# Optimization experiments

Measured on AMD Instinct MI355X. Metric: run time of the kernel, lower is better.

Reference implementation:

```python
import jax, jax.numpy as jnp
import numpy as np

B = 1024            # number of graphs
C = (64, 32, 16, 1) # args.channels
K = 25              # args.kernel_size
CUTOFF = 0.5        # args.cutoff
EPS = 1e-15


def gmm_conv(x, pos, n, g, mu, sigma, root, bias, out_ch):
    """GMMConv over a dynamically-built radius graph (dist<CUTOFF, no self loops),
    with mean aggregation, expressed densely per-graph (n in {5,25,75}).
    Equivalent to getA()+PyG GMMConv(aggr='mean') scatter/gather."""
    nb = pos.shape[0] // n
    posb = pos.reshape(nb, n, 2)
    # diff[b, s, t] = pos_t - pos_s  (edge (row=s, col=t): message flows s -> t)
    diff = posb[:, None, :, :] - posb[:, :, None, :]
    dist = jnp.linalg.norm(diff + 1e-12, axis=-1)            # [B,n,n]
    mask = (dist < CUTOFF) & (~jnp.eye(n, dtype=bool))       # [B,n,n]
    pseudo = diff / CUTOFF + 0.5                             # [B,n,n,2] edge_attr
    # Gaussian kernel weights: exp(-0.5 * sum_d (u_d - mu_kd)^2 / sigma_kd^2)
    gauss = jnp.exp(-0.5 * jnp.sum((pseudo[..., None, :] - mu) ** 2
                                   / (sigma ** 2 + EPS), axis=-1))  # [B,n,n,K]
    w = gauss * mask[..., None]
    xm = (x @ g).reshape(nb, n, K, out_ch)                   # source-transformed feats
    agg = jnp.einsum('bstk,bsko->bto', w, xm)                # scatter-sum into targets
    deg = jnp.maximum(jnp.sum(mask, axis=1), 1)              # in-degree per target [B,n]
    out = agg / deg[..., None].astype(x.dtype)               # mean aggregation
    return out.reshape(-1, out_ch) + x @ root + bias


def setup_inputs() -> dict:
    key = jax.random.key(0)
    ks = jax.random.split(key, 40)
    inp = {}
    inp['x'] = jax.random.normal(ks[0], (B * 5, C[0]), jnp.float32)
    inp['pos'] = jax.random.uniform(ks[1], (B * 5, 2), jnp.float32)

    def conv_params(k, fin, fout):
        k1, k2, k3, k4, k5 = jax.random.split(k, 5)
        g = jax.random.normal(k1, (fin, K * fout), jnp.float32) / np.sqrt(fin)
        mu = jax.random.normal(k2, (K, 2), jnp.float32)
        sigma = jax.random.uniform(k3, (K, 2), jnp.float32, minval=0.5, maxval=1.5)
        root = jax.random.normal(k4, (fin, fout), jnp.float32) / np.sqrt(fin)
        bias = jax.random.normal(k5, (fout,), jnp.float32) * 0.01
        return g, mu, sigma, root, bias

    for i, (fin, fout) in enumerate([(C[0], 5 * C[1]), (C[1], 3 * C[2]), (C[2], C[3])], 1):
        g, mu, sigma, root, bias = conv_params(ks[1 + i], fin, fout)
        inp[f'g{i}'], inp[f'mu{i}'], inp[f'sig{i}'] = g, mu, sigma
        inp[f'root{i}'], inp[f'cb{i}'] = root, bias

    def lin(k, fin, fout):
        kw, kb = jax.random.split(k)
        return (jax.random.normal(kw, (fin, fout), jnp.float32) / np.sqrt(fin),
                jax.random.normal(kb, (fout,), jnp.float32) * 0.01)

    for j, (pre, dims) in enumerate([('p1', (2 + C[1], 128, 64, 2)),
                                     ('p2', (2 + C[2], 128, 64, 2))]):
        for li in range(3):
            w, b_ = lin(ks[10 + 3 * j + li], dims[li], dims[li + 1])
            inp[f'{pre}w{li+1}'], inp[f'{pre}b{li+1}'] = w, b_
    return inp


def reference(x, pos, g1, mu1, sig1, root1, cb1, g2, mu2, sig2, root2, cb2,
              g3, mu3, sig3, root3, cb3,
              p1w1, p1b1, p1w2, p1b2, p1w3, p1b3,
              p2w1, p2b1, p2w2, p2b2, p2w3, p2b3):
    elu = jax.nn.elu
    # stage 1: 5 nodes/graph, conv expands node count x5
    x = elu(gmm_conv(x, pos, 5, g1, mu1, sig1, root1, cb1, 5 * C[1])).reshape(-1, C[1])
    p = jnp.concatenate([jnp.repeat(pos, 5, axis=0), x], axis=1)
    p = elu(p @ p1w1 + p1b1)
    p = elu(p @ p1w2 + p1b2)
    pos = elu(p @ p1w3 + p1b3)
    # stage 2: 25 nodes/graph, conv expands node count x3
    x = elu(gmm_conv(x, pos, 25, g2, mu2, sig2, root2, cb2, 3 * C[2])).reshape(-1, C[2])
    p = jnp.concatenate([jnp.repeat(pos, 3, axis=0), x], axis=1)
    p = elu(p @ p2w1 + p2b1)
    p = elu(p @ p2w2 + p2b2)
    pos = elu(p @ p2w3 + p2b3)
    # stage 3: 75 nodes/graph
    x = jnp.tanh(gmm_conv(x, pos, 75, g3, mu3, sig3, root3, cb3, C[3])).reshape(-1, C[3])
    return x, pos
```

## Files before the change

### kernel.cpp

```cpp
#include <hip/hip_runtime.h>
#include <math.h>


__device__ __forceinline__ float eluf(float v) { return v > 0.f ? v : __expf(v) - 1.f; }

#define NLOG2E_HALF (-0.72134752f)

__global__ __launch_bounds__(512) void conv1_kernel(
    const float* __restrict__ x, const float* __restrict__ pos,
    const float* __restrict__ g, const float* __restrict__ mu, const float* __restrict__ sig,
    const float* __restrict__ root, const float* __restrict__ bias,
    float* __restrict__ xout)
{
  const int b = blockIdx.x, tid = threadIdx.x;
  __shared__ __align__(16) float s_xT[64 * 12];
  __shared__ __align__(16) float s_xm[10 * 832];
  __shared__ __align__(16) float s_w[2 * 5 * 5 * 28];
  __shared__ __align__(16) float s_red[2 * 2 * 5 * 160];
  __shared__ float s_pos[20];
  __shared__ float s_msc[25][4];
  __shared__ float s_ideg[10];

  if (tid < 20) s_pos[tid] = pos[b * 20 + tid];
  if (tid < 25) {
    float m0 = mu[2 * tid], m1 = mu[2 * tid + 1];
    float s0 = sig[2 * tid], s1 = sig[2 * tid + 1];
    s_msc[tid][0] = 0.5f - m0;
    s_msc[tid][1] = 0.5f - m1;
    s_msc[tid][2] = NLOG2E_HALF / (s0 * s0 + 1e-15f);
    s_msc[tid][3] = NLOG2E_HALF / (s1 * s1 + 1e-15f);
  }
  for (int e = tid; e < 640; e += 512) { int nd = e >> 6, i = e & 63; s_xT[i * 12 + nd] = x[b * 640 + nd * 64 + i]; }
  for (int e = tid; e < 320; e += 512) { int r = e / 32, c = e % 32; s_xm[r * 832 + 800 + c] = 0.f; }
  __syncthreads();

  if (tid < 10) {
    int gg = tid / 5, t = tid % 5, c = 0;
    for (int s = 0; s < 5; ++s) {
      if (s == t) continue;
      float d0 = s_pos[(gg * 5 + t) * 2]     - s_pos[(gg * 5 + s) * 2]     + 1e-12f;
      float d1 = s_pos[(gg * 5 + t) * 2 + 1] - s_pos[(gg * 5 + s) * 2 + 1] + 1e-12f;
      c += (d0 * d0 + d1 * d1 < 0.25f) ? 1 : 0;
    }
    s_ideg[tid] = 1.f / (float)(c < 1 ? 1 : c);
  }
  for (int e = tid; e < 1400; e += 512) {
    int gg = e / 700, r2 = e % 700, t = r2 / 140, c = r2 % 140;
    int ch = c / 28, skl = c % 28;
    float wv = 0.f;
    if (skl < 25) {
      int kk = skl / 5, s = skl % 5, k = ch * 5 + kk;
      float d0 = s_pos[(gg * 5 + t) * 2]     - s_pos[(gg * 5 + s) * 2];
      float d1 = s_pos[(gg * 5 + t) * 2 + 1] - s_pos[(gg * 5 + s) * 2 + 1];
      float e0 = d0 + 1e-12f, e1 = d1 + 1e-12f;
      bool m = (e0 * e0 + e1 * e1 < 0.25f) && (s != t);
      float q0 = fmaf(2.f, d0, s_msc[k][0]);
      float q1 = fmaf(2.f, d1, s_msc[k][1]);
      float a = q0 * q0 * s_msc[k][2];
      a = fmaf(q1 * q1, s_msc[k][3], a);
      wv = m ? exp2f(a) : 0.f;
    }
    s_w[e] = wv;
  }
  __syncthreads();

  float sacc[5][2];
  #pragma unroll
  for (int t = 0; t < 5; ++t) { sacc[t][0] = 0.f; sacc[t][1] = 0.f; }
  const int sg = tid / 160, sr = tid % 160, sks = sr / 80, sob = sr % 80;
  const int so0 = sob * 2;

  for (int ch = 0; ch < 5; ++ch) {
    if (tid < 400) {
      const int c0 = tid * 2;
      const float* gp = g + ch * 800 + c0;
      float a[10][2];
      #pragma unroll
      for (int r = 0; r < 10; ++r) { a[r][0] = 0.f; a[r][1] = 0.f; }
      #pragma unroll 4
      for (int i = 0; i < 64; ++i) {
        float2 gv = *(const float2*)(gp + i * 4000);
        float4 xa = *(const float4*)&s_xT[i * 12];
        float4 xb = *(const float4*)&s_xT[i * 12 + 4];
        float2 xc = *(const float2*)&s_xT[i * 12 + 8];
        a[0][0] = fmaf(xa.x, gv.x, a[0][0]); a[0][1] = fmaf(xa.x, gv.y, a[0][1]);
        a[1][0] = fmaf(xa.y, gv.x, a[1][0]); a[1][1] = fmaf(xa.y, gv.y, a[1][1]);
        a[2][0] = fmaf(xa.z, gv.x, a[2][0]); a[2][1] = fmaf(xa.z, gv.y, a[2][1]);
        a[3][0] = fmaf(xa.w, gv.x, a[3][0]); a[3][1] = fmaf(xa.w, gv.y, a[3][1]);
        a[4][0] = fmaf(xb.x, gv.x, a[4][0]); a[4][1] = fmaf(xb.x, gv.y, a[4][1]);
        a[5][0] = fmaf(xb.y, gv.x, a[5][0]); a[5][1] = fmaf(xb.y, gv.y, a[5][1]);
        a[6][0] = fmaf(xb.z, gv.x, a[6][0]); a[6][1] = fmaf(xb.z, gv.y, a[6][1]);
        a[7][0] = fmaf(xb.w, gv.x, a[7][0]); a[7][1] = fmaf(xb.w, gv.y, a[7][1]);
        a[8][0] = fmaf(xc.x, gv.x, a[8][0]); a[8][1] = fmaf(xc.x, gv.y, a[8][1]);
        a[9][0] = fmaf(xc.y, gv.x, a[9][0]); a[9][1] = fmaf(xc.y, gv.y, a[9][1]);
      }
      #pragma unroll
      for (int r = 0; r < 10; ++r)
        *(float2*)&s_xm[r * 832 + c0] = make_float2(a[r][0], a[r][1]);
    }
    __syncthreads();
    if (tid < 320) {
#define C1_STEP(SK0) { \
      float2 m0 = *(const float2*)&s_xm[(sg * 5 + ((SK0) % 5)) * 832 + ((SK0) / 5) * 160 + so0]; \
      float2 m1 = *(const float2*)&s_xm[(sg * 5 + (((SK0) + 1) % 5)) * 832 + (((SK0) + 1) / 5) * 160 + so0]; \
      float2 m2 = *(const float2*)&s_xm[(sg * 5 + (((SK0) + 2) % 5)) * 832 + (((SK0) + 2) / 5) * 160 + so0]; \
      float2 m3 = *(const float2*)&s_xm[(sg * 5 + (((SK0) + 3) % 5)) * 832 + (((SK0) + 3) / 5) * 160 + so0]; \
      _Pragma("unroll") \
      for (int t = 0; t < 5; ++t) { \
        const float4 wv = *(const float4*)&s_w[((sg * 5 + t) * 5 + ch) * 28 + (SK0)]; \
        sacc[t][0] = fmaf(wv.x, m0.x, sacc[t][0]); sacc[t][1] = fmaf(wv.x, m0.y, sacc[t][1]); \
        sacc[t][0] = fmaf(wv.y, m1.x, sacc[t][0]); sacc[t][1] = fmaf(wv.y, m1.y, sacc[t][1]); \
        sacc[t][0] = fmaf(wv.z, m2.x, sacc[t][0]); sacc[t][1] = fmaf(wv.z, m2.y, sacc[t][1]); \
        sacc[t][0] = fmaf(wv.w, m3.x, sacc[t][0]); sacc[t][1] = fmaf(wv.w, m3.y, sacc[t][1]); \
      } }
      if (sks == 0) { C1_STEP(0) C1_STEP(4) C1_STEP(8) C1_STEP(12) }
      else          { C1_STEP(16) C1_STEP(20) C1_STEP(24) }
#undef C1_STEP
    }
    __syncthreads();
  }

  if (tid < 400) {
    const int rb = tid / 80, cb = tid % 80;
    const int r0 = rb * 2, c0 = cb * 2;
    float a00 = 0.f, a01 = 0.f, a10 = 0.f, a11 = 0.f;
    #pragma unroll 4
    for (int i = 0; i < 64; ++i) {
      float2 rv = *(const float2*)(root + i * 160 + c0);
      float2 xv = *(const float2*)&s_xT[i * 12 + r0];
      a00 = fmaf(xv.x, rv.x, a00); a01 = fmaf(xv.x, rv.y, a01);
      a10 = fmaf(xv.y, rv.x, a10); a11 = fmaf(xv.y, rv.y, a11);
    }
    *(float2*)&s_xm[r0 * 832 + c0]       = make_float2(a00, a01);
    *(float2*)&s_xm[(r0 + 1) * 832 + c0] = make_float2(a10, a11);
  }
  if (tid < 320) {
    #pragma unroll
    for (int t = 0; t < 5; ++t) {
      s_red[((sks * 2 + sg) * 5 + t) * 160 + so0]     = sacc[t][0];
      s_red[((sks * 2 + sg) * 5 + t) * 160 + so0 + 1] = sacc[t][1];
    }
  }
  __syncthreads();
  for (int e = tid; e < 1600; e += 512) {
    int gg = e / 800, r2 = e % 800, t = r2 / 160, o = r2 % 160;
    float v = s_red[(gg * 5 + t) * 160 + o] + s_red[((2 + gg) * 5 + t) * 160 + o];
    v = v * s_ideg[gg * 5 + t] + s_xm[(gg * 5 + t) * 832 + o] + bias[o];
    xout[b * 1600 + e] = eluf(v);
  }
}

__global__ __launch_bounds__(320) void conv2_kernel(
    const float* __restrict__ x, const float* __restrict__ pos,
    const float* __restrict__ g, const float* __restrict__ mu, const float* __restrict__ sig,
    const float* __restrict__ root, const float* __restrict__ bias,
    float* __restrict__ xout)
{
  const int b = blockIdx.x, tid = threadIdx.x;
  __shared__ __align__(16) float s_xT[32 * 28];
  __shared__ __align__(16) float s_xm[125 * 52];
  __shared__ __align__(16) float s_w[25 * 132];
  __shared__ __align__(8)  float2 s_u[25 * 26];
  __shared__ float s_ek[25 * 5];
  __shared__ float s_pos[50];
  __shared__ float s_ideg[25];

  if (tid < 50) s_pos[tid] = pos[b * 50 + tid];
  if (tid < 25) {
    float m0 = mu[2 * tid], m1 = mu[2 * tid + 1];
    float sg0 = sig[2 * tid], sg1 = sig[2 * tid + 1];
    float n0 = NLOG2E_HALF / (sg0 * sg0 + 1e-15f);
    float n1 = NLOG2E_HALF / (sg1 * sg1 + 1e-15f);
    float c0 = 0.5f - m0, c1 = 0.5f - m1;
    s_ek[tid * 5 + 0] = n0;
    s_ek[tid * 5 + 1] = n1;
    s_ek[tid * 5 + 2] = 2.f * n0 * c0;
    s_ek[tid * 5 + 3] = 2.f * n1 * c1;
    s_ek[tid * 5 + 4] = fmaf(n0, c0 * c0, n1 * c1 * c1);
  }
  for (int e = tid; e < 800; e += 320) { int r = e / 32, i = e % 32; s_xT[i * 28 + r] = x[b * 800 + e]; }
  __syncthreads();

  for (int e = tid; e < 625; e += 320) {
    int t = e / 25, s = e % 25;
    float d0 = s_pos[t * 2]     - s_pos[s * 2];
    float d1 = s_pos[t * 2 + 1] - s_pos[s * 2 + 1];
    float e0 = d0 + 1e-12f, e1 = d1 + 1e-12f;
    bool m = (e0 * e0 + e1 * e1 < 0.25f) && (s != t);
    s_u[t * 26 + s] = m ? make_float2(2.f * d0, 2.f * d1) : make_float2(1e18f, 0.f);
  }
  if (tid < 25) {
    int t = tid, c = 0;
    for (int s = 0; s < 25; ++s) {
      if (s == t) continue;
      float d0 = s_pos[t * 2]     - s_pos[s * 2]     + 1e-12f;
      float d1 = s_pos[t * 2 + 1] - s_pos[s * 2 + 1] + 1e-12f;
      c += (d0 * d0 + d1 * d1 < 0.25f) ? 1 : 0;
    }
    s_ideg[t] = 1.f / (float)(c < 1 ? 1 : c);
  }
  __syncthreads();

  const bool act = tid < 300;
  const int grp = tid / 60, rr = tid % 60, tg = rr / 12, og = rr % 12;
  const int o0 = og * 4;
  const int t0 = tg * 5, sk0 = grp * 25, s0 = tg * 5;

  float acc2[5][4];
  #pragma unroll
  for (int tt = 0; tt < 5; ++tt) { acc2[tt][0] = acc2[tt][1] = acc2[tt][2] = acc2[tt][3] = 0.f; }

  for (int ch = 0; ch < 5; ++ch) {
    const int k0 = ch * 5;
    for (int e = tid; e < 3125; e += 320) {
      int t = e / 125, c = e % 125;
      int kk = c / 25, s = c % 25, k = k0 + kk;
      float2 uv = s_u[t * 26 + s];
      const float* ekp = &s_ek[k * 5];
      float ar = fmaf(uv.x * uv.x, ekp[0],
                 fmaf(uv.y * uv.y, ekp[1],
                 fmaf(uv.x, ekp[2],
                 fmaf(uv.y, ekp[3], ekp[4]))));
      s_w[t * 132 + c] = exp2f(ar);
    }
    if (act) {
      const float* gp = g + (k0 + grp) * 48 + o0;
      float a[5][4];
      #pragma unroll
      for (int r = 0; r < 5; ++r) { a[r][0] = a[r][1] = a[r][2] = a[r][3] = 0.f; }
      #pragma unroll 4
      for (int i = 0; i < 32; ++i) {
        float4 gv = *(const float4*)(gp + i * 1200);
        float x0 = s_xT[i * 28 + s0];
        float x1 = s_xT[i * 28 + s0 + 1];
        float x2 = s_xT[i * 28 + s0 + 2];
        float x3 = s_xT[i * 28 + s0 + 3];
        float x4 = s_xT[i * 28 + s0 + 4];
        a[0][0] = fmaf(x0, gv.x, a[0][0]); a[0][1] = fmaf(x0, gv.y, a[0][1]);
        a[0][2] = fmaf(x0, gv.z, a[0][2]); a[0][3] = fmaf(x0, gv.w, a[0][3]);
        a[1][0] = fmaf(x1, gv.x, a[1][0]); a[1][1] = fmaf(x1, gv.y, a[1][1]);
        a[1][2] = fmaf(x1, gv.z, a[1][2]); a[1][3] = fmaf(x1, gv.w, a[1][3]);
        a[2][0] = fmaf(x2, gv.x, a[2][0]); a[2][1] = fmaf(x2, gv.y, a[2][1]);
        a[2][2] = fmaf(x2, gv.z, a[2][2]); a[2][3] = fmaf(x2, gv.w, a[2][3]);
        a[3][0] = fmaf(x3, gv.x, a[3][0]); a[3][1] = fmaf(x3, gv.y, a[3][1]);
        a[3][2] = fmaf(x3, gv.z, a[3][2]); a[3][3] = fmaf(x3, gv.w, a[3][3]);
        a[4][0] = fmaf(x4, gv.x, a[4][0]); a[4][1] = fmaf(x4, gv.y, a[4][1]);
        a[4][2] = fmaf(x4, gv.z, a[4][2]); a[4][3] = fmaf(x4, gv.w, a[4][3]);
      }
      #pragma unroll
      for (int j = 0; j < 5; ++j)
        *(float4*)&s_xm[(grp * 25 + s0 + j) * 52 + o0] = make_float4(a[j][0], a[j][1], a[j][2], a[j][3]);
    }
    __syncthreads();
    if (act) {
      #pragma unroll 5
      for (int q = 0; q < 25; ++q) {
        const int sk = sk0 + q;
        float4 mv = *(const float4*)&s_xm[sk * 52 + o0];
        float w0 = s_w[(t0 + 0) * 132 + sk];
        float w1 = s_w[(t0 + 1) * 132 + sk];
        float w2 = s_w[(t0 + 2) * 132 + sk];
        float w3 = s_w[(t0 + 3) * 132 + sk];
        float w4 = s_w[(t0 + 4) * 132 + sk];
        acc2[0][0] = fmaf(w0, mv.x, acc2[0][0]); acc2[0][1] = fmaf(w0, mv.y, acc2[0][1]);
        acc2[0][2] = fmaf(w0, mv.z, acc2[0][2]); acc2[0][3] = fmaf(w0, mv.w, acc2[0][3]);
        acc2[1][0] = fmaf(w1, mv.x, acc2[1][0]); acc2[1][1] = fmaf(w1, mv.y, acc2[1][1]);
        acc2[1][2] = fmaf(w1, mv.z, acc2[1][2]); acc2[1][3] = fmaf(w1, mv.w, acc2[1][3]);
        acc2[2][0] = fmaf(w2, mv.x, acc2[2][0]); acc2[2][1] = fmaf(w2, mv.y, acc2[2][1]);
        acc2[2][2] = fmaf(w2, mv.z, acc2[2][2]); acc2[2][3] = fmaf(w2, mv.w, acc2[2][3]);
        acc2[3][0] = fmaf(w3, mv.x, acc2[3][0]); acc2[3][1] = fmaf(w3, mv.y, acc2[3][1]);
        acc2[3][2] = fmaf(w3, mv.z, acc2[3][2]); acc2[3][3] = fmaf(w3, mv.w, acc2[3][3]);
        acc2[4][0] = fmaf(w4, mv.x, acc2[4][0]); acc2[4][1] = fmaf(w4, mv.y, acc2[4][1]);
        acc2[4][2] = fmaf(w4, mv.z, acc2[4][2]); acc2[4][3] = fmaf(w4, mv.w, acc2[4][3]);
      }
    }
    __syncthreads();
  }

  if (act) {
    #pragma unroll
    for (int tt = 0; tt < 5; ++tt)
      *(float4*)&s_xm[grp * 1200 + (t0 + tt) * 48 + o0] =
          make_float4(acc2[tt][0], acc2[tt][1], acc2[tt][2], acc2[tt][3]);
  }
  __syncthreads();
  for (int e = tid; e < 1200; e += 320) {
    int t = e / 48, o = e % 48;
    float v = s_xm[e] + s_xm[1200 + e] + s_xm[2400 + e] + s_xm[3600 + e] + s_xm[4800 + e];
    v *= s_ideg[t];
    #pragma unroll 8
    for (int i = 0; i < 32; ++i) v = fmaf(s_xT[i * 28 + t], root[i * 48 + o], v);
    xout[b * 1200 + e] = eluf(v + bias[o]);
  }
}

__global__ __launch_bounds__(384) void conv3_kernel(
    const float* __restrict__ x, const float* __restrict__ pos,
    const float* __restrict__ g, const float* __restrict__ mu, const float* __restrict__ sig,
    const float* __restrict__ root, const float* __restrict__ bias,
    float* __restrict__ xout)
{
  const int b = blockIdx.x, tid = threadIdx.x;
  __shared__ __align__(8) float2 s_u[75 * 75];
  __shared__ float s_xm[75 * 28];
  __shared__ float s_x[75 * 16];
  __shared__ float s_g3[400];
  __shared__ float s_pos[150];
  __shared__ float s_ek[25 * 5];
  __shared__ float s_ideg[75];
  __shared__ float s_out[75];
  __shared__ float s_r3[16];

  if (tid < 150) s_pos[tid] = pos[b * 150 + tid];
  for (int e = tid; e < 1200; e += 384) s_x[e] = x[b * 1200 + e];
  for (int e = tid; e < 400; e += 384) s_g3[e] = g[e];
  if (tid < 25) {
    float m0 = mu[2 * tid], m1 = mu[2 * tid + 1];
    float sg0 = sig[2 * tid], sg1 = sig[2 * tid + 1];
    float n0 = NLOG2E_HALF / (sg0 * sg0 + 1e-15f);
    float n1 = NLOG2E_HALF / (sg1 * sg1 + 1e-15f);
    float c0 = 0.5f - m0, c1 = 0.5f - m1;
    s_ek[tid * 5 + 0] = n0;
    s_ek[tid * 5 + 1] = n1;
    s_ek[tid * 5 + 2] = 2.f * n0 * c0;
    s_ek[tid * 5 + 3] = 2.f * n1 * c1;
    s_ek[tid * 5 + 4] = n0 * c0 * c0 + n1 * c1 * c1;
  }
  if (tid < 16) s_r3[tid] = root[tid];
  if (tid < 75) s_out[tid] = 0.f;
  __syncthreads();

  for (int e = tid; e < 1875; e += 384) {
    int s = e / 25, k = e % 25;
    float a = 0.f;
    #pragma unroll
    for (int i = 0; i < 16; ++i) a = fmaf(s_x[s * 16 + i], s_g3[i * 25 + k], a);
    s_xm[s * 28 + k] = a;
  }
  for (int e = tid; e < 5625; e += 384) {
    int t = e / 75, s = e % 75;
    float d0 = s_pos[t * 2]     - s_pos[s * 2];
    float d1 = s_pos[t * 2 + 1] - s_pos[s * 2 + 1];
    float e0 = d0 + 1e-12f, e1 = d1 + 1e-12f;
    bool m = (e0 * e0 + e1 * e1 < 0.25f) && (s != t);
    s_u[e] = m ? make_float2(2.f * d0, 2.f * d1) : make_float2(1e18f, 0.f);
  }
  if (tid < 75) {
    int t = tid, c = 0;
    for (int s = 0; s < 75; ++s) {
      if (s == t) continue;
      float d0 = s_pos[t * 2]     - s_pos[s * 2]     + 1e-12f;
      float d1 = s_pos[t * 2 + 1] - s_pos[s * 2 + 1] + 1e-12f;
      c += (d0 * d0 + d1 * d1 < 0.25f) ? 1 : 0;
    }
    s_ideg[t] = 1.f / (float)(c < 1 ? 1 : c);
  }
  __syncthreads();

  if (tid < 375) {
    const int t = tid / 5, kg = tid % 5;
    float n0[5], n1[5], e0[5], e1[5], f[5];
    #pragma unroll
    for (int j = 0; j < 5; ++j) {
      int k = kg * 5 + j;
      n0[j] = s_ek[k * 5 + 0]; n1[j] = s_ek[k * 5 + 1];
      e0[j] = s_ek[k * 5 + 2]; e1[j] = s_ek[k * 5 + 3];
      f[j]  = s_ek[k * 5 + 4];
    }
    float acc[5] = {0.f, 0.f, 0.f, 0.f, 0.f};
    for (int s = 0; s < 75; ++s) {
      float2 uv = s_u[t * 75 + s];
      float u00 = uv.x * uv.x, u11 = uv.y * uv.y;
      #pragma unroll
      for (int j = 0; j < 5; ++j) {
        float ar = fmaf(u00, n0[j], fmaf(u11, n1[j], fmaf(uv.x, e0[j], fmaf(uv.y, e1[j], f[j]))));
        acc[j] = fmaf(exp2f(ar), s_xm[s * 28 + kg * 5 + j], acc[j]);
      }
    }
    float sum = acc[0] + acc[1] + acc[2] + acc[3] + acc[4];
    atomicAdd(&s_out[t], sum);
  }
  __syncthreads();

  if (tid < 75) {
    int t = tid;
    float r = 0.f;
    #pragma unroll
    for (int i = 0; i < 16; ++i) r = fmaf(s_x[t * 16 + i], s_r3[i], r);
    xout[b * 75 + t] = tanhf(s_out[t] * s_ideg[t] + r + bias[0]);
  }
}

__global__ __launch_bounds__(256) void mlp_kernel(
    const float* __restrict__ pos_src, const float* __restrict__ feat,
    const float* __restrict__ w1, const float* __restrict__ b1,
    const float* __restrict__ w2, const float* __restrict__ b2,
    const float* __restrict__ w3, const float* __restrict__ b3,
    float* __restrict__ out, int fdim, int rep)
{
  const int tid = threadIdx.x;
  const int row0 = blockIdx.x * 64;
  const int din = fdim + 2;
  __shared__ __align__(16) float s_inT[34][68];
  __shared__ __align__(16) float s_h1T[128][68];
  __shared__ __align__(16) float s_h2T[64][68];

  if (tid < 128) {
    int r = tid >> 1, d = tid & 1;
    s_inT[d][r] = pos_src[((row0 + r) / rep) * 2 + d];
  }
  for (int e = tid; e < 64 * fdim; e += 256) {
    int r = e / fdim, c = e % fdim;
    s_inT[2 + c][r] = feat[(row0 + r) * fdim + c];
  }
  __syncthreads();

  {
    const int rb = tid >> 4, jb = tid & 15;
    const int r0 = rb << 2, j0 = jb << 3;
    float acc[4][8];
    #pragma unroll
    for (int jj = 0; jj < 8; ++jj) {
      float bv = b1[j0 + jj];
      acc[0][jj] = bv; acc[1][jj] = bv; acc[2][jj] = bv; acc[3][jj] = bv;
    }
    for (int i = 0; i < din; ++i) {
      float4 xa = *(const float4*)&s_inT[i][r0];
      float4 wa = *(const float4*)(w1 + i * 128 + j0);
      float4 wb = *(const float4*)(w1 + i * 128 + j0 + 4);
      float wv[8] = {wa.x, wa.y, wa.z, wa.w, wb.x, wb.y, wb.z, wb.w};
      #pragma unroll
      for (int jj = 0; jj < 8; ++jj) {
        acc[0][jj] = fmaf(xa.x, wv[jj], acc[0][jj]);
        acc[1][jj] = fmaf(xa.y, wv[jj], acc[1][jj]);
        acc[2][jj] = fmaf(xa.z, wv[jj], acc[2][jj]);
        acc[3][jj] = fmaf(xa.w, wv[jj], acc[3][jj]);
      }
    }
    #pragma unroll
    for (int jj = 0; jj < 8; ++jj)
      *(float4*)&s_h1T[j0 + jj][r0] =
        make_float4(eluf(acc[0][jj]), eluf(acc[1][jj]), eluf(acc[2][jj]), eluf(acc[3][jj]));
  }
  __syncthreads();

  {
    const int rb = tid >> 4, jb = tid & 15;
    const int r0 = rb << 2, j0 = jb << 2;
    float acc[4][4];
    #pragma unroll
    for (int jj = 0; jj < 4; ++jj) {
      float bv = b2[j0 + jj];
      acc[0][jj] = bv; acc[1][jj] = bv; acc[2][jj] = bv; acc[3][jj] = bv;
    }
    #pragma unroll 4
    for (int i = 0; i < 128; ++i) {
      float4 ha = *(const float4*)&s_h1T[i][r0];
      float4 wa = *(const float4*)(w2 + i * 64 + j0);
      float wv[4] = {wa.x, wa.y, wa.z, wa.w};
      #pragma unroll
      for (int jj = 0; jj < 4; ++jj) {
        acc[0][jj] = fmaf(ha.x, wv[jj], acc[0][jj]);
        acc[1][jj] = fmaf(ha.y, wv[jj], acc[1][jj]);
        acc[2][jj] = fmaf(ha.z, wv[jj], acc[2][jj]);
        acc[3][jj] = fmaf(ha.w, wv[jj], acc[3][jj]);
      }
    }
    #pragma unroll
    for (int jj = 0; jj < 4; ++jj)
      *(float4*)&s_h2T[j0 + jj][r0] =
        make_float4(eluf(acc[0][jj]), eluf(acc[1][jj]), eluf(acc[2][jj]), eluf(acc[3][jj]));
  }
  __syncthreads();

  if (tid < 128) {
    int r = tid >> 1, c = tid & 1;
    float a = b3[c];
    #pragma unroll 8
    for (int j = 0; j < 64; ++j)
      a = fmaf(s_h2T[j][r], w3[j * 2 + c], a);
    out[(row0 + r) * 2 + c] = eluf(a);
  }
}

extern "C" void kernel_launch(void* const* d_in, const int* in_sizes, int n_in,
                              void* d_out, int out_size, void* d_ws, size_t ws_size,
                              hipStream_t stream)
{
  const float* x     = (const float*)d_in[0];
  const float* pos   = (const float*)d_in[1];
  const float* g1    = (const float*)d_in[2];
  const float* mu1   = (const float*)d_in[3];
  const float* sig1  = (const float*)d_in[4];
  const float* root1 = (const float*)d_in[5];
  const float* cb1   = (const float*)d_in[6];
  const float* g2    = (const float*)d_in[7];
  const float* mu2   = (const float*)d_in[8];
  const float* sig2  = (const float*)d_in[9];
  const float* root2 = (const float*)d_in[10];
  const float* cb2   = (const float*)d_in[11];
  const float* g3    = (const float*)d_in[12];
  const float* mu3   = (const float*)d_in[13];
  const float* sig3  = (const float*)d_in[14];
  const float* root3 = (const float*)d_in[15];
  const float* cb3   = (const float*)d_in[16];
  const float* p1w1  = (const float*)d_in[17];
  const float* p1b1  = (const float*)d_in[18];
  const float* p1w2  = (const float*)d_in[19];
  const float* p1b2  = (const float*)d_in[20];
  const float* p1w3  = (const float*)d_in[21];
  const float* p1b3  = (const float*)d_in[22];
  const float* p2w1  = (const float*)d_in[23];
  const float* p2b1  = (const float*)d_in[24];
  const float* p2w2  = (const float*)d_in[25];
  const float* p2b2  = (const float*)d_in[26];
  const float* p2w3  = (const float*)d_in[27];
  const float* p2b3  = (const float*)d_in[28];

  float* out  = (float*)d_out;
  float* ws   = (float*)d_ws;
  float* x1   = ws;
  float* pos1 = ws + 819200;
  float* x2   = ws + 870400;
  float* x3   = out;
  float* pos2 = out + 76800;

  conv1_kernel<<<dim3(512), dim3(512), 0, stream>>>(x, pos, g1, mu1, sig1, root1, cb1, x1);
  mlp_kernel<<<dim3(400), dim3(256), 0, stream>>>(pos, x1, p1w1, p1b1, p1w2, p1b2, p1w3, p1b3,
                                                  pos1, 32, 5);
  conv2_kernel<<<dim3(1024), dim3(320), 0, stream>>>(x1, pos1, g2, mu2, sig2, root2, cb2, x2);
  mlp_kernel<<<dim3(1200), dim3(256), 0, stream>>>(pos1, x2, p2w1, p2b1, p2w2, p2b2, p2w3, p2b3,
                                                  pos2, 16, 3);
  conv3_kernel<<<dim3(1024), dim3(384), 0, stream>>>(x2, pos2, g3, mu3, sig3, root3, cb3, x3);
}
```

Measured before the change: 336.6 us.

## Restructure conv1/conv2 tiling, warp-specialize conv2 weights, halve MLP rows per block

conv1 now keeps x row-major with padding and each thread computes a 5x4 output tile, loading g as float4. conv2 grows to 512 threads and splits them by role: some threads do the source transform while the others compute Gaussian weights concurrently. The aggregation is re-tiled over source-kernel chunks, with partial sums merged through shared-memory atomics. The MLP kernel processes 32 rows per block in a smaller aliased shared buffer to raise occupancy and block count, at the cost of reloading weights more often and adding atomic contention in conv2.

Result: slower. 589.0 us (+75.0%).

```diff
diff --git a/kernel.cpp b/kernel.cpp
--- a/kernel.cpp
+++ b/kernel.cpp
@@ -5,6 +5,10 @@
 __device__ __forceinline__ float eluf(float v) { return v > 0.f ? v : __expf(v) - 1.f; }
 
 #define NLOG2E_HALF (-0.72134752f)
+
+#define FMA4(A, S, V) \
+  A.x = fmaf(S, V.x, A.x); A.y = fmaf(S, V.y, A.y); \
+  A.z = fmaf(S, V.z, A.z); A.w = fmaf(S, V.w, A.w);
 
 __global__ __launch_bounds__(512) void conv1_kernel(
     const float* __restrict__ x, const float* __restrict__ pos,
@@ -13,7 +17,7 @@
     float* __restrict__ xout)
 {
   const int b = blockIdx.x, tid = threadIdx.x;
-  __shared__ __align__(16) float s_xT[64 * 12];
+  __shared__ __align__(16) float s_x[10 * 68];
   __shared__ __align__(16) float s_xm[10 * 832];
   __shared__ __align__(16) float s_w[2 * 5 * 5 * 28];
   __shared__ __align__(16) float s_red[2 * 2 * 5 * 160];
@@ -30,7 +34,7 @@
     s_msc[tid][2] = NLOG2E_HALF / (s0 * s0 + 1e-15f);
     s_msc[tid][3] = NLOG2E_HALF / (s1 * s1 + 1e-15f);
   }
-  for (int e = tid; e < 640; e += 512) { int nd = e >> 6, i = e & 63; s_xT[i * 12 + nd] = x[b * 640 + nd * 64 + i]; }
+  for (int e = tid; e < 640; e += 512) { int nd = e >> 6, i = e & 63; s_x[nd * 68 + i] = x[b * 640 + e]; }
   for (int e = tid; e < 320; e += 512) { int r = e / 32, c = e % 32; s_xm[r * 832 + 800 + c] = 0.f; }
   __syncthreads();
 
@@ -70,33 +74,35 @@
   const int sg = tid / 160, sr = tid % 160, sks = sr / 80, sob = sr % 80;
   const int so0 = sob * 2;
 
+#define C1G(J, XV) \
+  a[J][0]=fmaf(XV.x,gv0.x,a[J][0]); a[J][1]=fmaf(XV.x,gv0.y,a[J][1]); a[J][2]=fmaf(XV.x,gv0.z,a[J][2]); a[J][3]=fmaf(XV.x,gv0.w,a[J][3]); \
+  a[J][0]=fmaf(XV.y,gv1.x,a[J][0]); a[J][1]=fmaf(XV.y,gv1.y,a[J][1]); a[J][2]=fmaf(XV.y,gv1.z,a[J][2]); a[J][3]=fmaf(XV.y,gv1.w,a[J][3]); \
+  a[J][0]=fmaf(XV.z,gv2.x,a[J][0]); a[J][1]=fmaf(XV.z,gv2.y,a[J][1]); a[J][2]=fmaf(XV.z,gv2.z,a[J][2]); a[J][3]=fmaf(XV.z,gv2.w,a[J][3]); \
+  a[J][0]=fmaf(XV.w,gv3.x,a[J][0]); a[J][1]=fmaf(XV.w,gv3.y,a[J][1]); a[J][2]=fmaf(XV.w,gv3.z,a[J][2]); a[J][3]=fmaf(XV.w,gv3.w,a[J][3]);
+
   for (int ch = 0; ch < 5; ++ch) {
     if (tid < 400) {
-      const int c0 = tid * 2;
+      const int gg = tid / 200, c0 = (tid % 200) * 4;
       const float* gp = g + ch * 800 + c0;
-      float a[10][2];
-      #pragma unroll
-      for (int r = 0; r < 10; ++r) { a[r][0] = 0.f; a[r][1] = 0.f; }
-      #pragma unroll 4
-      for (int i = 0; i < 64; ++i) {
-        float2 gv = *(const float2*)(gp + i * 4000);
-        float4 xa = *(const float4*)&s_xT[i * 12];
-        float4 xb = *(const float4*)&s_xT[i * 12 + 4];
-        float2 xc = *(const float2*)&s_xT[i * 12 + 8];
-        a[0][0] = fmaf(xa.x, gv.x, a[0][0]); a[0][1] = fmaf(xa.x, gv.y, a[0][1]);
-        a[1][0] = fmaf(xa.y, gv.x, a[1][0]); a[1][1] = fmaf(xa.y, gv.y, a[1][1]);
-        a[2][0] = fmaf(xa.z, gv.x, a[2][0]); a[2][1] = fmaf(xa.z, gv.y, a[2][1]);
-        a[3][0] = fmaf(xa.w, gv.x, a[3][0]); a[3][1] = fmaf(xa.w, gv.y, a[3][1]);
-        a[4][0] = fmaf(xb.x, gv.x, a[4][0]); a[4][1] = fmaf(xb.x, gv.y, a[4][1]);
-        a[5][0] = fmaf(xb.y, gv.x, a[5][0]); a[5][1] = fmaf(xb.y, gv.y, a[5][1]);
-        a[6][0] = fmaf(xb.z, gv.x, a[6][0]); a[6][1] = fmaf(xb.z, gv.y, a[6][1]);
-        a[7][0] = fmaf(xb.w, gv.x, a[7][0]); a[7][1] = fmaf(xb.w, gv.y, a[7][1]);
-        a[8][0] = fmaf(xc.x, gv.x, a[8][0]); a[8][1] = fmaf(xc.x, gv.y, a[8][1]);
-        a[9][0] = fmaf(xc.y, gv.x, a[9][0]); a[9][1] = fmaf(xc.y, gv.y, a[9][1]);
-      }
-      #pragma unroll
-      for (int r = 0; r < 10; ++r)
-        *(float2*)&s_xm[r * 832 + c0] = make_float2(a[r][0], a[r][1]);
+      const float* xb = &s_x[gg * 5 * 68];
+      float a[5][4];
+      #pragma unroll
+      for (int r = 0; r < 5; ++r) { a[r][0] = a[r][1] = a[r][2] = a[r][3] = 0.f; }
+      for (int i = 0; i < 64; i += 4) {
+        float4 gv0 = *(const float4*)(gp + (i + 0) * 4000);
+        float4 gv1 = *(const float4*)(gp + (i + 1) * 4000);
+        float4 gv2 = *(const float4*)(gp + (i + 2) * 4000);
+        float4 gv3 = *(const float4*)(gp + (i + 3) * 4000);
+        float4 xv0 = *(const float4*)(xb + 0 * 68 + i);
+        float4 xv1 = *(const float4*)(xb + 1 * 68 + i);
+        float4 xv2 = *(const float4*)(xb + 2 * 68 + i);
+        float4 xv3 = *(const float4*)(xb + 3 * 68 + i);
+        float4 xv4 = *(const float4*)(xb + 4 * 68 + i);
+        C1G(0, xv0) C1G(1, xv1) C1G(2, xv2) C1G(3, xv3) C1G(4, xv4)
+      }
+      #pragma unroll
+      for (int r = 0; r < 5; ++r)
+        *(float4*)&s_xm[(gg * 5 + r) * 832 + c0] = make_float4(a[r][0], a[r][1], a[r][2], a[r][3]);
     }
     __syncthreads();
     if (tid < 320) {
@@ -121,18 +127,27 @@
   }
 
   if (tid < 400) {
-    const int rb = tid / 80, cb = tid % 80;
-    const int r0 = rb * 2, c0 = cb * 2;
+    const int rg = tid / 80, og = tid % 80;
+    const int r0 = rg * 2, o0 = og * 2;
     float a00 = 0.f, a01 = 0.f, a10 = 0.f, a11 = 0.f;
-    #pragma unroll 4
-    for (int i = 0; i < 64; ++i) {
-      float2 rv = *(const float2*)(root + i * 160 + c0);
-      float2 xv = *(const float2*)&s_xT[i * 12 + r0];
-      a00 = fmaf(xv.x, rv.x, a00); a01 = fmaf(xv.x, rv.y, a01);
-      a10 = fmaf(xv.y, rv.x, a10); a11 = fmaf(xv.y, rv.y, a11);
-    }
-    *(float2*)&s_xm[r0 * 832 + c0]       = make_float2(a00, a01);
-    *(float2*)&s_xm[(r0 + 1) * 832 + c0] = make_float2(a10, a11);
+    for (int i = 0; i < 64; i += 4) {
+      float4 x0 = *(const float4*)&s_x[r0 * 68 + i];
+      float4 x1 = *(const float4*)&s_x[(r0 + 1) * 68 + i];
+      float2 rv0 = *(const float2*)(root + (i + 0) * 160 + o0);
+      float2 rv1 = *(const float2*)(root + (i + 1) * 160 + o0);
+      float2 rv2 = *(const float2*)(root + (i + 2) * 160 + o0);
+      float2 rv3 = *(const float2*)(root + (i + 3) * 160 + o0);
+      a00 = fmaf(x0.x, rv0.x, a00); a01 = fmaf(x0.x, rv0.y, a01);
+      a10 = fmaf(x1.x, rv0.x, a10); a11 = fmaf(x1.x, rv0.y, a11);
+      a00 = fmaf(x0.y, rv1.x, a00); a01 = fmaf(x0.y, rv1.y, a01);
+      a10 = fmaf(x1.y, rv1.x, a10); a11 = fmaf(x1.y, rv1.y, a11);
+      a00 = fmaf(x0.z, rv2.x, a00); a01 = fmaf(x0.z, rv2.y, a01);
+      a10 = fmaf(x1.z, rv2.x, a10); a11 = fmaf(x1.z, rv2.y, a11);
+      a00 = fmaf(x0.w, rv3.x, a00); a01 = fmaf(x0.w, rv3.y, a01);
+      a10 = fmaf(x1.w, rv3.x, a10); a11 = fmaf(x1.w, rv3.y, a11);
+    }
+    *(float2*)&s_xm[r0 * 832 + o0]       = make_float2(a00, a01);
+    *(float2*)&s_xm[(r0 + 1) * 832 + o0] = make_float2(a10, a11);
   }
   if (tid < 320) {
     #pragma unroll
@@ -150,22 +165,24 @@
   }
 }
 
-__global__ __launch_bounds__(320) void conv2_kernel(
+__global__ __launch_bounds__(512) void conv2_kernel(
     const float* __restrict__ x, const float* __restrict__ pos,
     const float* __restrict__ g, const float* __restrict__ mu, const float* __restrict__ sig,
     const float* __restrict__ root, const float* __restrict__ bias,
     float* __restrict__ xout)
 {
   const int b = blockIdx.x, tid = threadIdx.x;
-  __shared__ __align__(16) float s_xT[32 * 28];
+  __shared__ __align__(16) float s_x[25 * 36];
   __shared__ __align__(16) float s_xm[125 * 52];
-  __shared__ __align__(16) float s_w[25 * 132];
+  __shared__ __align__(16) float s_w[5 * 125 * 8];
   __shared__ __align__(8)  float2 s_u[25 * 26];
+  __shared__ float s_out[25 * 48];
   __shared__ float s_ek[25 * 5];
-  __shared__ float s_pos[50];
   __shared__ float s_ideg[25];
 
-  if (tid < 50) s_pos[tid] = pos[b * 50 + tid];
+  const float* posb = pos + b * 50;
+  for (int e = tid; e < 800; e += 512) s_x[(e / 32) * 36 + (e % 32)] = x[b * 800 + e];
+  for (int e = tid; e < 1200; e += 512) s_out[e] = 0.f;
   if (tid < 25) {
     float m0 = mu[2 * tid], m1 = mu[2 * tid + 1];
     float sg0 = sig[2 * tid], sg1 = sig[2 * tid + 1];
@@ -178,13 +195,10 @@
     s_ek[tid * 5 + 3] = 2.f * n1 * c1;
     s_ek[tid * 5 + 4] = fmaf(n0, c0 * c0, n1 * c1 * c1);
   }
-  for (int e = tid; e < 800; e += 320) { int r = e / 32, i = e % 32; s_xT[i * 28 + r] = x[b * 800 + e]; }
-  __syncthreads();
-
-  for (int e = tid; e < 625; e += 320) {
+  for (int e = tid; e < 625; e += 512) {
     int t = e / 25, s = e % 25;
-    float d0 = s_pos[t * 2]     - s_pos[s * 2];
-    float d1 = s_pos[t * 2 + 1] - s_pos[s * 2 + 1];
+    float d0 = posb[t * 2]     - posb[s * 2];
+    float d1 = posb[t * 2 + 1] - posb[s * 2 + 1];
     float e0 = d0 + 1e-12f, e1 = d1 + 1e-12f;
     bool m = (e0 * e0 + e1 * e1 < 0.25f) && (s != t);
     s_u[t * 26 + s] = m ? make_float2(2.f * d0, 2.f * d1) : make_float2(1e18f, 0.f);
@@ -193,104 +207,118 @@
     int t = tid, c = 0;
     for (int s = 0; s < 25; ++s) {
       if (s == t) continue;
-      float d0 = s_pos[t * 2]     - s_pos[s * 2]     + 1e-12f;
-      float d1 = s_pos[t * 2 + 1] - s_pos[s * 2 + 1] + 1e-12f;
+      float d0 = posb[t * 2]     - posb[s * 2]     + 1e-12f;
+      float d1 = posb[t * 2 + 1] - posb[s * 2 + 1] + 1e-12f;
       c += (d0 * d0 + d1 * d1 < 0.25f) ? 1 : 0;
     }
     s_ideg[t] = 1.f / (float)(c < 1 ? 1 : c);
   }
   __syncthreads();
 
-  const bool act = tid < 300;
-  const int grp = tid / 60, rr = tid % 60, tg = rr / 12, og = rr % 12;
-  const int o0 = og * 4;
-  const int t0 = tg * 5, sk0 = grp * 25, s0 = tg * 5;
-
-  float acc2[5][4];
+  const int g_kk = tid / 60, g_sg = (tid / 12) % 5, g_og = tid % 12;
+  const int s_grp = tid / 15, s_tile = tid % 15;
+  const int s_tg = s_tile / 3, s_og = s_tile % 3;
+  const int s_t0 = s_tg * 5, s_o0 = s_og * 16;
+
+  float4 acc4[5][4];
   #pragma unroll
-  for (int tt = 0; tt < 5; ++tt) { acc2[tt][0] = acc2[tt][1] = acc2[tt][2] = acc2[tt][3] = 0.f; }
+  for (int j = 0; j < 5; ++j)
+    #pragma unroll
+    for (int q = 0; q < 4; ++q) acc4[j][q] = make_float4(0.f, 0.f, 0.f, 0.f);
 
   for (int ch = 0; ch < 5; ++ch) {
     const int k0 = ch * 5;
-    for (int e = tid; e < 3125; e += 320) {
-      int t = e / 125, c = e % 125;
-      int kk = c / 25, s = c % 25, k = k0 + kk;
-      float2 uv = s_u[t * 26 + s];
-      const float* ekp = &s_ek[k * 5];
-      float ar = fmaf(uv.x * uv.x, ekp[0],
-                 fmaf(uv.y * uv.y, ekp[1],
-                 fmaf(uv.x, ekp[2],
-                 fmaf(uv.y, ekp[3], ekp[4]))));
-      s_w[t * 132 + c] = exp2f(ar);
-    }
-    if (act) {
-      const float* gp = g + (k0 + grp) * 48 + o0;
+    if (tid < 300) {
+      const int s0 = g_sg * 5, o0 = g_og * 4;
+      const float* gp = g + (k0 + g_kk) * 48 + o0;
+      const float* xb = &s_x[s0 * 36];
       float a[5][4];
       #pragma unroll
       for (int r = 0; r < 5; ++r) { a[r][0] = a[r][1] = a[r][2] = a[r][3] = 0.f; }
-      #pragma unroll 4
-      for (int i = 0; i < 32; ++i) {
-        float4 gv = *(const float4*)(gp + i * 1200);
-        float x0 = s_xT[i * 28 + s0];
-        float x1 = s_xT[i * 28 + s0 + 1];
-        float x2 = s_xT[i * 28 + s0 + 2];
-        float x3 = s_xT[i * 28 + s0 + 3];
-        float x4 = s_xT[i * 28 + s0 + 4];
-        a[0][0] = fmaf(x0, gv.x, a[0][0]); a[0][1] = fmaf(x0, gv.y, a[0][1]);
-        a[0][2] = fmaf(x0, gv.z, a[0][2]); a[0][3] = fmaf(x0, gv.w, a[0][3]);
-        a[1][0] = fmaf(x1, gv.x, a[1][0]); a[1][1] = fmaf(x1, gv.y, a[1][1]);
-        a[1][2] = fmaf(x1, gv.z, a[1][2]); a[1][3] = fmaf(x1, gv.w, a[1][3]);
-        a[2][0] = fmaf(x2, gv.x, a[2][0]); a[2][1] = fmaf(x2, gv.y, a[2][1]);
-        a[2][2] = fmaf(x2, gv.z, a[2][2]); a[2][3] = fmaf(x2, gv.w, a[2][3]);
-        a[3][0] = fmaf(x3, gv.x, a[3][0]); a[3][1] = fmaf(x3, gv.y, a[3][1]);
-        a[3][2] = fmaf(x3, gv.z, a[3][2]); a[3][3] = fmaf(x3, gv.w, a[3][3]);
-        a[4][0] = fmaf(x4, gv.x, a[4][0]); a[4][1] = fmaf(x4, gv.y, a[4][1]);
-        a[4][2] = fmaf(x4, gv.z, a[4][2]); a[4][3] = fmaf(x4, gv.w, a[4][3]);
+      for (int i = 0; i < 32; i += 4) {
+        float4 gv0 = *(const float4*)(gp + (i + 0) * 1200);
+        float4 gv1 = *(const float4*)(gp + (i + 1) * 1200);
+        float4 gv2 = *(const float4*)(gp + (i + 2) * 1200);
+        float4 gv3 = *(const float4*)(gp + (i + 3) * 1200);
+        float4 xv0 = *(const float4*)(xb + 0 * 36 + i);
+        float4 xv1 = *(const float4*)(xb + 1 * 36 + i);
+        float4 xv2 = *(const float4*)(xb + 2 * 36 + i);
+        float4 xv3 = *(const float4*)(xb + 3 * 36 + i);
+        float4 xv4 = *(const float4*)(xb + 4 * 36 + i);
+        C1G(0, xv0) C1G(1, xv1) C1G(2, xv2) C1G(3, xv3) C1G(4, xv4)
       }
       #pragma unroll
       for (int j = 0; j < 5; ++j)
-        *(float4*)&s_xm[(grp * 25 + s0 + j) * 52 + o0] = make_float4(a[j][0], a[j][1], a[j][2], a[j][3]);
+        *(float4*)&s_xm[(g_kk * 25 + s0 + j) * 52 + o0] = make_float4(a[j][0], a[j][1], a[j][2], a[j][3]);
+    } else if (tid >= 320) {
+      for (int e = tid - 320; e < 3125; e += 192) {
+        int t = e / 125, r = e % 125;
+        int kk = r / 25, s = r % 25, k = k0 + kk;
+        float2 uv = s_u[t * 26 + s];
+        const float* ekp = &s_ek[k * 5];
+        float ar = fmaf(uv.x * uv.x, ekp[0],
+                   fmaf(uv.y * uv.y, ekp[1],
+                   fmaf(uv.x, ekp[2],
+                   fmaf(uv.y, ekp[3], ekp[4]))));
+        s_w[(t / 5) * 1000 + (kk * 25 + s) * 8 + (t % 5)] = exp2f(ar);
+      }
     }
     __syncthreads();
-    if (act) {
-      #pragma unroll 5
-      for (int q = 0; q < 25; ++q) {
-        const int sk = sk0 + q;
-        float4 mv = *(const float4*)&s_xm[sk * 52 + o0];
-        float w0 = s_w[(t0 + 0) * 132 + sk];
-        float w1 = s_w[(t0 + 1) * 132 + sk];
-        float w2 = s_w[(t0 + 2) * 132 + sk];
-        float w3 = s_w[(t0 + 3) * 132 + sk];
-        float w4 = s_w[(t0 + 4) * 132 + sk];
-        acc2[0][0] = fmaf(w0, mv.x, acc2[0][0]); acc2[0][1] = fmaf(w0, mv.y, acc2[0][1]);
-        acc2[0][2] = fmaf(w0, mv.z, acc2[0][2]); acc2[0][3] = fmaf(w0, mv.w, acc2[0][3]);
-        acc2[1][0] = fmaf(w1, mv.x, acc2[1][0]); acc2[1][1] = fmaf(w1, mv.y, acc2[1][1]);
-        acc2[1][2] = fmaf(w1, mv.z, acc2[1][2]); acc2[1][3] = fmaf(w1, mv.w, acc2[1][3]);
-        acc2[2][0] = fmaf(w2, mv.x, acc2[2][0]); acc2[2][1] = fmaf(w2, mv.y, acc2[2][1]);
-        acc2[2][2] = fmaf(w2, mv.z, acc2[2][2]); acc2[2][3] = fmaf(w2, mv.w, acc2[2][3]);
-        acc2[3][0] = fmaf(w3, mv.x, acc2[3][0]); acc2[3][1] = fmaf(w3, mv.y, acc2[3][1]);
-        acc2[3][2] = fmaf(w3, mv.z, acc2[3][2]); acc2[3][3] = fmaf(w3, mv.w, acc2[3][3]);
-        acc2[4][0] = fmaf(w4, mv.x, acc2[4][0]); acc2[4][1] = fmaf(w4, mv.y, acc2[4][1]);
-        acc2[4][2] = fmaf(w4, mv.z, acc2[4][2]); acc2[4][3] = fmaf(w4, mv.w, acc2[4][3]);
+    if (tid < 510) {
+      const int skend = (s_grp * 4 + 4 < 125) ? s_grp * 4 + 4 : 125;
+      for (int sk = s_grp * 4; sk < skend; ++sk) {
+        const float* wp = &s_w[s_tg * 1000 + sk * 8];
+        float4 w4 = *(const float4*)wp;
+        float wx = wp[4];
+        float wj[5] = {w4.x, w4.y, w4.z, w4.w, wx};
+        const float* mp = &s_xm[sk * 52 + s_o0];
+        float4 m0 = *(const float4*)(mp);
+        float4 m1 = *(const float4*)(mp + 4);
+        float4 m2 = *(const float4*)(mp + 8);
+        float4 m3 = *(const float4*)(mp + 12);
+        #pragma unroll
+        for (int j = 0; j < 5; ++j) {
+          FMA4(acc4[j][0], wj[j], m0)
+          FMA4(acc4[j][1], wj[j], m1)
+          FMA4(acc4[j][2], wj[j], m2)
+          FMA4(acc4[j][3], wj[j], m3)
+        }
       }
     }
     __syncthreads();
   }
 
-  if (act) {
-    #pragma unroll
-    for (int tt = 0; tt < 5; ++tt)
-      *(float4*)&s_xm[grp * 1200 + (t0 + tt) * 48 + o0] =
-          make_float4(acc2[tt][0], acc2[tt][1], acc2[tt][2], acc2[tt][3]);
-  }
-  __syncthreads();
-  for (int e = tid; e < 1200; e += 320) {
-    int t = e / 48, o = e % 48;
-    float v = s_xm[e] + s_xm[1200 + e] + s_xm[2400 + e] + s_xm[3600 + e] + s_xm[4800 + e];
-    v *= s_ideg[t];
-    #pragma unroll 8
-    for (int i = 0; i < 32; ++i) v = fmaf(s_xT[i * 28 + t], root[i * 48 + o], v);
-    xout[b * 1200 + e] = eluf(v + bias[o]);
+  if (tid < 510) {
+    #pragma unroll
+    for (int j = 0; j < 5; ++j) {
+      #pragma unroll
+      for (int q = 0; q < 4; ++q) {
+        float* dst = &s_out[(s_t0 + j) * 48 + s_o0 + q * 4];
+        float4 v = acc4[j][q];
+        atomicAdd(dst + 0, v.x);
+        atomicAdd(dst + 1, v.y);
+        atomicAdd(dst + 2, v.z);
+        atomicAdd(dst + 3, v.w);
+      }
+    }
+  }
+  __syncthreads();
+
+  if (tid < 300) {
+    const int t = tid / 12, o0 = (tid % 12) * 4;
+    float4 bv = *(const float4*)&bias[o0];
+    float4 sv = *(const float4*)&s_out[t * 48 + o0];
+    float idg = s_ideg[t];
+    float4 v = make_float4(fmaf(sv.x, idg, bv.x), fmaf(sv.y, idg, bv.y),
+                           fmaf(sv.z, idg, bv.z), fmaf(sv.w, idg, bv.w));
+    const float* xr = &s_x[t * 36];
+    for (int i = 0; i < 32; ++i) {
+      float4 rv = *(const float4*)(root + i * 48 + o0);
+      float xv = xr[i];
+      FMA4(v, xv, rv)
+    }
+    *(float4*)&xout[b * 1200 + t * 48 + o0] =
+        make_float4(eluf(v.x), eluf(v.y), eluf(v.z), eluf(v.w));
   }
 }
 
@@ -399,67 +427,67 @@
     float* __restrict__ out, int fdim, int rep)
 {
   const int tid = threadIdx.x;
-  const int row0 = blockIdx.x * 64;
+  const int row0 = blockIdx.x * 32;
   const int din = fdim + 2;
-  __shared__ __align__(16) float s_inT[34][68];
-  __shared__ __align__(16) float s_h1T[128][68];
-  __shared__ __align__(16) float s_h2T[64][68];
-
-  if (tid < 128) {
+  __shared__ __align__(16) char smem[27648];
+  float* s_h1T = (float*)smem;
+  float* s_inT = (float*)(smem + 18432);
+  float* s_h2T = (float*)(smem + 18432);
+
+  if (tid < 64) {
     int r = tid >> 1, d = tid & 1;
-    s_inT[d][r] = pos_src[((row0 + r) / rep) * 2 + d];
-  }
-  for (int e = tid; e < 64 * fdim; e += 256) {
+    s_inT[d * 36 + r] = pos_src[((row0 + r) / rep) * 2 + d];
+  }
+  for (int e = tid; e < 32 * fdim; e += 256) {
     int r = e / fdim, c = e % fdim;
-    s_inT[2 + c][r] = feat[(row0 + r) * fdim + c];
-  }
-  __syncthreads();
-
+    s_inT[(2 + c) * 36 + r] = feat[(row0 + r) * fdim + c];
+  }
+  __syncthreads();
+
+  const int rb = tid / 32, jb = tid % 32;
   {
-    const int rb = tid >> 4, jb = tid & 15;
-    const int r0 = rb << 2, j0 = jb << 3;
-    float acc[4][8];
-    #pragma unroll
-    for (int jj = 0; jj < 8; ++jj) {
+    const int r0 = rb * 4, j0 = jb * 4;
+    float acc[4][4];
+    #pragma unroll
+    for (int jj = 0; jj < 4; ++jj) {
       float bv = b1[j0 + jj];
       acc[0][jj] = bv; acc[1][jj] = bv; acc[2][jj] = bv; acc[3][jj] = bv;
     }
     for (int i = 0; i < din; ++i) {
-      float4 xa = *(const float4*)&s_inT[i][r0];
-      float4 wa = *(const float4*)(w1 + i * 128 + j0);
-      float4 wb = *(const float4*)(w1 + i * 128 + j0 + 4);
-      float wv[8] = {wa.x, wa.y, wa.z, wa.w, wb.x, wb.y, wb.z, wb.w};
-      #pragma unroll
-      for (int jj = 0; jj < 8; ++jj) {
+      float4 xa = *(const float4*)&s_inT[i * 36 + r0];
+      float4 wa = *(const float4*)&w1[i * 128 + j0];
+      float wv[4] = {wa.x, wa.y, wa.z, wa.w};
+      #pragma unroll
+      for (int jj = 0; jj < 4; ++jj) {
         acc[0][jj] = fmaf(xa.x, wv[jj], acc[0][jj]);
         acc[1][jj] = fmaf(xa.y, wv[jj], acc[1][jj]);
         acc[2][jj] = fmaf(xa.z, wv[jj], acc[2][jj]);
         acc[3][jj] = fmaf(xa.w, wv[jj], acc[3][jj]);
       }
     }
-    #pragma unroll
-    for (int jj = 0; jj < 8; ++jj)
-      *(float4*)&s_h1T[j0 + jj][r0] =
+    __syncthreads();
+    #pragma unroll
+    for (int jj = 0; jj < 4; ++jj)
+      *(float4*)&s_h1T[(j0 + jj) * 36 + r0] =
         make_float4(eluf(acc[0][jj]), eluf(acc[1][jj]), eluf(acc[2][jj]), eluf(acc[3][jj]));
   }
   __syncthreads();
 
   {
-    const int rb = tid >> 4, jb = tid & 15;
-    const int r0 = rb << 2, j0 = jb << 2;
-    float acc[4][4];
-    #pragma unroll
-    for (int jj = 0; jj < 4; ++jj) {
+    const int r0 = rb * 4, j0 = jb * 2;
+    float acc[4][2];
+    #pragma unroll
+    for (int jj = 0; jj < 2; ++jj) {
       float bv = b2[j0 + jj];
       acc[0][jj] = bv; acc[1][jj] = bv; acc[2][jj] = bv; acc[3][jj] = bv;
     }
     #pragma unroll 4
     for (int i = 0; i < 128; ++i) {
-      float4 ha = *(const float4*)&s_h1T[i][r0];
-      float4 wa = *(const float4*)(w2 + i * 64 + j0);
-      float wv[4] = {wa.x, wa.y, wa.z, wa.w};
-      #pragma unroll
-      for (int jj = 0; jj < 4; ++jj) {
+      float4 ha = *(const float4*)&s_h1T[i * 36 + r0];
+      float2 wa = *(const float2*)&w2[i * 64 + j0];
+      float wv[2] = {wa.x, wa.y};
+      #pragma unroll
+      for (int jj = 0; jj < 2; ++jj) {
         acc[0][jj] = fmaf(ha.x, wv[jj], acc[0][jj]);
         acc[1][jj] = fmaf(ha.y, wv[jj], acc[1][jj]);
         acc[2][jj] = fmaf(ha.z, wv[jj], acc[2][jj]);
@@ -467,18 +495,18 @@
       }
     }
     #pragma unroll
-    for (int jj = 0; jj < 4; ++jj)
-      *(float4*)&s_h2T[j0 + jj][r0] =
+    for (int jj = 0; jj < 2; ++jj)
+      *(float4*)&s_h2T[(j0 + jj) * 36 + r0] =
         make_float4(eluf(acc[0][jj]), eluf(acc[1][jj]), eluf(acc[2][jj]), eluf(acc[3][jj]));
   }
   __syncthreads();
 
-  if (tid < 128) {
+  if (tid < 64) {
     int r = tid >> 1, c = tid & 1;
     float a = b3[c];
     #pragma unroll 8
     for (int j = 0; j < 64; ++j)
-      a = fmaf(s_h2T[j][r], w3[j * 2 + c], a);
+      a = fmaf(s_h2T[j * 36 + r], w3[j * 2 + c], a);
     out[(row0 + r) * 2 + c] = eluf(a);
   }
 }
@@ -526,10 +554,10 @@
   float* pos2 = out + 76800;
 
   conv1_kernel<<<dim3(512), dim3(512), 0, stream>>>(x, pos, g1, mu1, sig1, root1, cb1, x1);
-  mlp_kernel<<<dim3(400), dim3(256), 0, stream>>>(pos, x1, p1w1, p1b1, p1w2, p1b2, p1w3, p1b3,
+  mlp_kernel<<<dim3(800), dim3(256), 0, stream>>>(pos, x1, p1w1, p1b1, p1w2, p1b2, p1w3, p1b3,
                                                   pos1, 32, 5);
-  conv2_kernel<<<dim3(1024), dim3(320), 0, stream>>>(x1, pos1, g2, mu2, sig2, root2, cb2, x2);
-  mlp_kernel<<<dim3(1200), dim3(256), 0, stream>>>(pos1, x2, p2w1, p2b1, p2w2, p2b2, p2w3, p2b3,
+  conv2_kernel<<<dim3(1024), dim3(512), 0, stream>>>(x1, pos1, g2, mu2, sig2, root2, cb2, x2);
+  mlp_kernel<<<dim3(2400), dim3(256), 0, stream>>>(pos1, x2, p2w1, p2b1, p2w2, p2b2, p2w3, p2b3,
                                                   pos2, 16, 3);
   conv3_kernel<<<dim3(1024), dim3(384), 0, stream>>>(x2, pos2, g3, mu3, sig3, root3, cb3, x3);
 }
```
